# Optimization experiments

Measured on AMD Instinct MI355X. Metric: run time of the kernel, lower is better.

## Reference

```python
import jax, jax.numpy as jnp
import numpy as np

DIM = 2048
N_HEADS = 16
N_KV_HEADS = 4
HEAD_DIM = 128
EPS = 1e-6
BS, SEQ = 2, 4096


def setup_inputs() -> dict:
    key = jax.random.key(0)
    ks = jax.random.split(key, 8)
    x = jax.random.normal(ks[0], (BS, SEQ, DIM), dtype=jnp.float32)
    # rotary freqs: unit-modulus complex represented as [seq, head_dim//2, 2]
    theta = 10000.0
    inv_freq = 1.0 / (theta ** (jnp.arange(0, HEAD_DIM, 2, dtype=jnp.float32) / HEAD_DIM))
    t = jnp.arange(SEQ, dtype=jnp.float32)
    ang = jnp.outer(t, inv_freq)  # [SEQ, HEAD_DIM//2]
    freqs_cis = jnp.stack([jnp.cos(ang), jnp.sin(ang)], axis=-1)  # [SEQ, HD/2, 2]
    std = 0.02
    wq = jax.random.normal(ks[1], (N_HEADS * HEAD_DIM, DIM), dtype=jnp.float32) * std
    wk = jax.random.normal(ks[2], (N_KV_HEADS * HEAD_DIM, DIM), dtype=jnp.float32) * std
    wv = jax.random.normal(ks[3], (N_KV_HEADS * HEAD_DIM, DIM), dtype=jnp.float32) * std
    wo = jax.random.normal(ks[4], (DIM, N_HEADS * HEAD_DIM), dtype=jnp.float32) * std
    q_norm_w = jnp.ones((HEAD_DIM,), dtype=jnp.float32)
    k_norm_w = jnp.ones((HEAD_DIM,), dtype=jnp.float32)
    return {"x": x, "freqs_cis": freqs_cis, "wq": wq, "wk": wk, "wv": wv,
            "wo": wo, "q_norm_w": q_norm_w, "k_norm_w": k_norm_w}


def _rms_norm(x, w, eps=EPS):
    xf = x.astype(jnp.float32)
    var = jnp.mean(xf * xf, axis=-1, keepdims=True)
    return w * (xf * jax.lax.rsqrt(var + eps)).astype(x.dtype)


def _apply_rope(x, freqs_cis):
    # x: [b, s, h, d]; freqs_cis: [s, d//2, 2] (cos, sin)
    b, s, h, d = x.shape
    xr = x.astype(jnp.float32).reshape(b, s, h, d // 2, 2)
    cos = freqs_cis[:s, :, 0][None, :, None, :]
    sin = freqs_cis[:s, :, 1][None, :, None, :]
    xre, xim = xr[..., 0], xr[..., 1]
    out = jnp.stack([xre * cos - xim * sin, xre * sin + xim * cos], axis=-1)
    return out.reshape(b, s, h, d).astype(x.dtype)


def reference(x, freqs_cis, wq, wk, wv, wo, q_norm_w, k_norm_w):
    bs, seqlen, _ = x.shape
    xq = jnp.einsum('bsd,ed->bse', x, wq).reshape(bs, seqlen, N_HEADS, HEAD_DIM)
    xk = jnp.einsum('bsd,ed->bse', x, wk).reshape(bs, seqlen, N_KV_HEADS, HEAD_DIM)
    xv = jnp.einsum('bsd,ed->bse', x, wv).reshape(bs, seqlen, N_KV_HEADS, HEAD_DIM)
    xq = _rms_norm(xq, q_norm_w)
    xk = _rms_norm(xk, k_norm_w)
    xq = _apply_rope(xq, freqs_cis)
    xk = _apply_rope(xk, freqs_cis)
    n_rep = N_HEADS // N_KV_HEADS
    # repeat_kv: [b,s,kvh,d] -> [b,s,kvh*n_rep,d]
    keys = jnp.repeat(xk, n_rep, axis=2)
    values = jnp.repeat(xv, n_rep, axis=2)
    q = xq.transpose(0, 2, 1, 3)  # [b,h,s,d]
    k = keys.transpose(0, 2, 1, 3)
    v = values.transpose(0, 2, 1, 3)
    scale = 1.0 / jnp.sqrt(jnp.asarray(HEAD_DIM, dtype=q.dtype))
    scores = jnp.einsum('bhqd,bhkd->bhqk', q, k) * scale
    causal = jnp.tril(jnp.ones((seqlen, seqlen), dtype=bool))
    scores = jnp.where(causal[None, None], scores, jnp.finfo(scores.dtype).min)
    attn = jax.nn.softmax(scores, axis=-1)
    out = jnp.einsum('bhqk,bhkd->bhqd', attn, v)
    out = out.transpose(0, 2, 1, 3).reshape(bs, seqlen, N_HEADS * HEAD_DIM)
    return jnp.einsum('bse,de->bsd', out, wo)
```

## Files before the change

### kernel.cpp

```cpp
#include <hip/hip_runtime.h>

typedef __bf16 bf16;
typedef __bf16 bf16x8 __attribute__((ext_vector_type(8)));
typedef __bf16 bf16x4 __attribute__((ext_vector_type(4)));
typedef __bf16 bf16x2 __attribute__((ext_vector_type(2)));
typedef float  f32x4  __attribute__((ext_vector_type(4)));

static_assert(sizeof(bf16x8) == 16, "bf16x8 must be 16B");

#define MFMA16(a, b, c) __builtin_amdgcn_mfma_f32_16x16x32_bf16((a), (b), (c), 0, 0, 0)

__device__ __forceinline__ void gload_lds16(const void* g, void* l) {
    __builtin_amdgcn_global_load_lds(
        (const __attribute__((address_space(1))) void*)(uintptr_t)g,
        (__attribute__((address_space(3))) void*)(uintptr_t)l,
        16, 0, 0);
}

__device__ __forceinline__ void cast8(const float* __restrict__ in, bf16* __restrict__ out, int i)
{
    const float4 a = ((const float4*)in)[i * 2];
    const float4 b = ((const float4*)in)[i * 2 + 1];
    bf16x8 o;
    o[0] = (bf16)a.x; o[1] = (bf16)a.y; o[2] = (bf16)a.z; o[3] = (bf16)a.w;
    o[4] = (bf16)b.x; o[5] = (bf16)b.y; o[6] = (bf16)b.z; o[7] = (bf16)b.w;
    ((bf16x8*)out)[i] = o;
}

__global__ __launch_bounds__(256)
void cast_all(const float* __restrict__ x,  const float* __restrict__ wq,
              const float* __restrict__ wk, const float* __restrict__ wv,
              bf16* __restrict__ xb, bf16* __restrict__ wb)
{
    const int blk = blockIdx.x;
    if (blk < 8192) {
        cast8(x, xb, blk * 256 + threadIdx.x);
    } else if (blk < 10240) {
        cast8(wq, wb, (blk - 8192) * 256 + threadIdx.x);
    } else if (blk < 10752) {
        cast8(wk, wb + 2048 * 2048, (blk - 10240) * 256 + threadIdx.x);
    } else {
        cast8(wv, wb + 2560 * 2048, (blk - 10752) * 256 + threadIdx.x);
    }
}

template <typename OT, bool FUSE_VT>
__global__ __launch_bounds__(256)
void gemm_bt(const bf16* __restrict__ A, const bf16* __restrict__ W,
             int K, int ldc, OT* __restrict__ C, bf16* __restrict__ vTp)
{
    __shared__ bf16 smem[2 * 128 * 64];
    bf16* As = smem;
    bf16* Bs = smem + 128 * 64;

    const int n0 = blockIdx.x * 128;
    const int m0 = blockIdx.y * 128;

    const int tid  = threadIdx.x;
    const int lane = tid & 63;
    const int wid  = tid >> 6;
    const int wm   = wid >> 1;
    const int wn   = wid & 1;
    const int quad = lane >> 4;
    const int l16  = lane & 15;
    const int key  = l16 & 7;

    const int srow  = wid * 32 + (lane >> 3);
    const int scolg = ((lane & 7) ^ (lane >> 3)) * 8;
    const bf16* ag = A + (size_t)(m0 + srow) * K + scolg;
    const bf16* wg = W + (size_t)(n0 + srow) * K + scolg;
    bf16* al = As + wid * 2048;
    bf16* bl = Bs + wid * 2048;

    f32x4 acc[4][4];
#pragma unroll
    for (int i = 0; i < 4; i++)
#pragma unroll
        for (int j = 0; j < 4; j++) acc[i][j] = f32x4{0.f, 0.f, 0.f, 0.f};

    for (int kt = 0; kt < K; kt += 64) {
        __syncthreads();
#pragma unroll
        for (int i = 0; i < 4; i++) {
            gload_lds16(ag + (size_t)(i * 8) * K, al + i * 8 * 64);
            gload_lds16(wg + (size_t)(i * 8) * K, bl + i * 8 * 64);
        }
        ag += 64; wg += 64;
        __syncthreads();

#pragma unroll
        for (int ks = 0; ks < 2; ks++) {
            bf16x8 af[4], bfv[4];
#pragma unroll
            for (int i = 0; i < 4; i++)
                af[i]  = *(const bf16x8*)(As + (wm * 64 + i * 16 + l16) * 64 + (((ks * 4 + quad) ^ key) * 8));
#pragma unroll
            for (int i = 0; i < 4; i++)
                bfv[i] = *(const bf16x8*)(Bs + (wn * 64 + i * 16 + l16) * 64 + (((ks * 4 + quad) ^ key) * 8));
#pragma unroll
            for (int mi = 0; mi < 4; mi++)
#pragma unroll
                for (int ni = 0; ni < 4; ni++)
                    acc[mi][ni] = MFMA16(af[mi], bfv[ni], acc[mi][ni]);
        }
    }

    if (FUSE_VT && n0 >= 2560) {
        __syncthreads();
        bf16* T = smem;
#pragma unroll
        for (int mi = 0; mi < 4; mi++) {
            const int scol = wm * 64 + mi * 16 + quad * 4;
            const int g    = scol >> 3;
            const int sub  = scol & 7;
#pragma unroll
            for (int ni = 0; ni < 4; ni++) {
                const int d = wn * 64 + ni * 16 + l16;
                bf16x4 h4;
                h4[0] = (bf16)acc[mi][ni][0]; h4[1] = (bf16)acc[mi][ni][1];
                h4[2] = (bf16)acc[mi][ni][2]; h4[3] = (bf16)acc[mi][ni][3];
                *(bf16x4*)(&T[d * 128 + ((g ^ (d & 7)) * 8 + sub)]) = h4;
            }
        }
        __syncthreads();
        const int kvh = (n0 - 2560) >> 7;
        const int bb  = m0 >> 12;
        bf16* vdst = vTp + ((size_t)((bb * 4 + kvh) * 128)) * 4096 + (m0 & 4095);
#pragma unroll
        for (int i = 0; i < 8; i++) {
            const int d = wid * 32 + i * 4 + quad;
            const bf16x8 v = *(const bf16x8*)(&T[d * 128 + ((l16 ^ (d & 7)) * 8)]);
            *(bf16x8*)(vdst + (size_t)d * 4096 + l16 * 8) = v;
        }
        return;
    }

#pragma unroll
    for (int mi = 0; mi < 4; mi++) {
        const int row = m0 + wm * 64 + mi * 16 + quad * 4;
#pragma unroll
        for (int ni = 0; ni < 4; ni++) {
            const int col = n0 + wn * 64 + ni * 16 + l16;
#pragma unroll
            for (int r = 0; r < 4; r++)
                C[(size_t)(row + r) * ldc + col] = (OT)acc[mi][ni][r];
        }
    }
}

__global__ __launch_bounds__(256)
void normrope_wo(bf16* __restrict__ qkv, const float* __restrict__ fc,
                 const float* __restrict__ qw, const float* __restrict__ kw,
                 const float* __restrict__ wo, bf16* __restrict__ wob)
{
    if (blockIdx.x >= 40960) {
        cast8(wo, wob, (blockIdx.x - 40960) * 256 + threadIdx.x);
        return;
    }
    const int row  = blockIdx.x * 4 + (threadIdx.x >> 6);
    const int lane = threadIdx.x & 63;
    const int slot = row % 20;
    const int tok  = row / 20;
    const int s    = tok & 4095;

    const float* w; int off; float post;
    if (slot < 16) { off = slot * 128;               w = qw; post = 0.12751681555f; }
    else           { off = 2048 + (slot - 16) * 128; w = kw; post = 1.0f; }

    bf16* p = qkv + (size_t)tok * 3072 + off;

    bf16x2 v = *(const bf16x2*)(p + 2 * lane);
    float x0 = (float)v[0], x1 = (float)v[1];

    float ss = x0 * x0 + x1 * x1;
    ss += __shfl_xor(ss, 1);  ss += __shfl_xor(ss, 2);  ss += __shfl_xor(ss, 4);
    ss += __shfl_xor(ss, 8);  ss += __shfl_xor(ss, 16); ss += __shfl_xor(ss, 32);
    const float r = rsqrtf(ss * (1.0f / 128.0f) + 1e-6f) * post;

    const float xn0 = x0 * r * w[2 * lane], xn1 = x1 * r * w[2 * lane + 1];

    const float2 cs = ((const float2*)fc)[(size_t)s * 64 + lane];
    const float c = cs.x, sn = cs.y;

    bf16x2 o;
    o[0] = (bf16)(xn0 * c - xn1 * sn);
    o[1] = (bf16)(xn0 * sn + xn1 * c);
    *(bf16x2*)(p + 2 * lane) = o;
}

__global__ __launch_bounds__(256, 2)
void flash(const bf16* __restrict__ qkv, const bf16* __restrict__ vT,
           bf16* __restrict__ out)
{
    const int flat = blockIdx.y * 16 + blockIdx.x;
    const int xcd  = flat & 7;
    const int idx  = flat >> 3;
    const int b    = xcd >> 2;
    const int kvh  = xcd & 3;
    const int h    = kvh * 4 + (idx >> 4);
    const int bx   = idx & 15;

    const int tid  = threadIdx.x;
    const int lane = tid & 63;
    const int wid  = tid >> 6;
    const int quad = lane >> 4;
    const int l16  = lane & 15;
    const int key  = l16 & 7;

    __shared__ bf16 Ks[2][64 * 128];
    __shared__ bf16 Vs[128 * 64];
    __shared__ bf16 Ps[128 * 64];

    const bf16* kbase = qkv + (size_t)b * 4096 * 3072 + 2048 + kvh * 128;
    const bf16* vbase = vT + ((size_t)(b * 4 + kvh) * 128) * 4096;

    const int krow_off = lane >> 4;
    const int kcolg    = lane & 15;
    const int vrow_off = lane >> 3;
    const int vcolg    = lane & 7;

    for (int pass = 0; pass < 2; ++pass) {
        const int qt = pass ? (31 - bx) : bx;
        const int q0 = qt * 128;
        const int ntiles = qt * 2 + 2;

        __syncthreads();
#pragma unroll
        for (int i = 0; i < 4; i++) {
            const int r0 = wid * 16 + i * 4;
            const int rk = r0 + krow_off;
            const int gc = (kcolg ^ (rk & 7)) * 8;
            gload_lds16(kbase + (size_t)rk * 3072 + gc, &Ks[0][r0 * 128]);
        }

        bf16x8 qf[2][4];
        const bf16* qbase = qkv + ((size_t)(b * 4096 + q0 + wid * 32)) * 3072 + h * 128;
#pragma unroll
        for (int mt = 0; mt < 2; mt++)
#pragma unroll
            for (int ks = 0; ks < 4; ks++)
                qf[mt][ks] = *(const bf16x8*)(qbase + (size_t)(mt * 16 + l16) * 3072 + ks * 32 + quad * 8);

        f32x4 oacc[2][8];
#pragma unroll
        for (int mt = 0; mt < 2; mt++)
#pragma unroll
            for (int nd = 0; nd < 8; nd++) oacc[mt][nd] = f32x4{0.f, 0.f, 0.f, 0.f};
        float mrow[2], lrow[2];
#pragma unroll
        for (int mt = 0; mt < 2; mt++) { mrow[mt] = -__builtin_inff(); lrow[mt] = 0.f; }

        __syncthreads();

#pragma unroll
        for (int i = 0; i < 4; i++) {
            const int r0 = wid * 32 + i * 8;
            const int dv = r0 + vrow_off;
            const int gc = (vcolg ^ (dv & 7)) * 8;
            gload_lds16(vbase + (size_t)dv * 4096 + gc, &Vs[r0 * 64]);
        }
#pragma unroll
        for (int i = 0; i < 4; i++) {
            const int r0 = wid * 16 + i * 4;
            const int rk = r0 + krow_off;
            const int gc = (kcolg ^ (rk & 7)) * 8;
            gload_lds16(kbase + (size_t)(64 + rk) * 3072 + gc, &Ks[1][r0 * 128]);
        }

        f32x4 sA[2][4], sB[2][4];

        {
#pragma unroll
            for (int mt = 0; mt < 2; mt++)
#pragma unroll
                for (int nt = 0; nt < 4; nt++) sA[mt][nt] = f32x4{0.f, 0.f, 0.f, 0.f};
            __builtin_amdgcn_s_setprio(1);
#pragma unroll
            for (int ks = 0; ks < 4; ks++) {
                bf16x8 kf[4];
#pragma unroll
                for (int nt = 0; nt < 4; nt++)
                    kf[nt] = *(const bf16x8*)(&Ks[0][(nt * 16 + l16) * 128 + (((ks * 4 + quad) ^ key) * 8)]);
#pragma unroll
                for (int mt = 0; mt < 2; mt++)
#pragma unroll
                    for (int nt = 0; nt < 4; nt++)
                        sA[mt][nt] = MFMA16(kf[nt], qf[mt][ks], sA[mt][nt]);
            }
            __builtin_amdgcn_s_setprio(0);
        }

        auto step = [&](int t, f32x4 (&SA)[2][4], f32x4 (&SB)[2][4]) {
            const int kv0 = t * 64;

            if (kv0 + 63 > q0) {
#pragma unroll
                for (int mt = 0; mt < 2; mt++) {
                    const int qg = q0 + wid * 32 + mt * 16 + l16;
#pragma unroll
                    for (int nt = 0; nt < 4; nt++)
#pragma unroll
                        for (int r = 0; r < 4; r++) {
                            const int kvg = kv0 + nt * 16 + quad * 4 + r;
                            if (kvg > qg) SA[mt][nt][r] = -1e30f;
                        }
                }
            }

            float pm[2];
#pragma unroll
            for (int mt = 0; mt < 2; mt++) {
                float t8[8];
#pragma unroll
                for (int nt = 0; nt < 4; nt++) {
                    t8[2 * nt]     = fmaxf(SA[mt][nt][0], SA[mt][nt][1]);
                    t8[2 * nt + 1] = fmaxf(SA[mt][nt][2], SA[mt][nt][3]);
                }
                float m = fmaxf(fmaxf(fmaxf(t8[0], t8[1]), fmaxf(t8[2], t8[3])),
                                fmaxf(fmaxf(t8[4], t8[5]), fmaxf(t8[6], t8[7])));
                m = fmaxf(m, __shfl_xor(m, 16));
                m = fmaxf(m, __shfl_xor(m, 32));
                pm[mt] = m;
            }

            const bool rescale =
                !__all((pm[0] - mrow[0] <= 8.f) && (pm[1] - mrow[1] <= 8.f));
            if (rescale) {
#pragma unroll
                for (int mt = 0; mt < 2; mt++) {
                    const float mnew  = fmaxf(mrow[mt], pm[mt]);
                    const float alpha = exp2f(mrow[mt] - mnew);
                    mrow[mt] = mnew;
                    lrow[mt] *= alpha;
                    float ar[4];
#pragma unroll
                    for (int r = 0; r < 4; r++) ar[r] = __shfl(alpha, quad * 4 + r);
#pragma unroll
                    for (int nd = 0; nd < 8; nd++)
#pragma unroll
                        for (int r = 0; r < 4; r++) oacc[mt][nd][r] *= ar[r];
                }
            }

#pragma unroll
            for (int mt = 0; mt < 2; mt++) {
                const int prow = wid * 32 + mt * 16 + l16;
                float sn[4];
#pragma unroll
                for (int nt = 0; nt < 4; nt++) {
                    const float p0 = exp2f(SA[mt][nt][0] - mrow[mt]);
                    const float p1 = exp2f(SA[mt][nt][1] - mrow[mt]);
                    const float p2 = exp2f(SA[mt][nt][2] - mrow[mt]);
                    const float p3 = exp2f(SA[mt][nt][3] - mrow[mt]);
                    sn[nt] = (p0 + p1) + (p2 + p3);
                    bf16x4 h4;
                    h4[0] = (bf16)p0; h4[1] = (bf16)p1;
                    h4[2] = (bf16)p2; h4[3] = (bf16)p3;
                    const int g = (2 * nt + (quad >> 1)) ^ key;
                    *(bf16x4*)(&Ps[prow * 64 + g * 8 + (quad & 1) * 4]) = h4;
                }
                float s = (sn[0] + sn[1]) + (sn[2] + sn[3]);
                s += __shfl_xor(s, 16);
                s += __shfl_xor(s, 32);
                lrow[mt] += s;
            }

            __syncthreads();

            if (t + 1 < ntiles) {
#pragma unroll
                for (int mt = 0; mt < 2; mt++)
#pragma unroll
                    for (int nt = 0; nt < 4; nt++) SB[mt][nt] = f32x4{0.f, 0.f, 0.f, 0.f};
                __builtin_amdgcn_s_setprio(1);
#pragma unroll
                for (int ks = 0; ks < 4; ks++) {
                    bf16x8 kf[4];
#pragma unroll
                    for (int nt = 0; nt < 4; nt++)
                        kf[nt] = *(const bf16x8*)(&Ks[(t + 1) & 1][(nt * 16 + l16) * 128 + (((ks * 4 + quad) ^ key) * 8)]);
#pragma unroll
                    for (int mt = 0; mt < 2; mt++)
#pragma unroll
                        for (int nt = 0; nt < 4; nt++)
                            SB[mt][nt] = MFMA16(kf[nt], qf[mt][ks], SB[mt][nt]);
                }
                __builtin_amdgcn_s_setprio(0);
            }

            __builtin_amdgcn_s_setprio(1);
#pragma unroll
            for (int ks = 0; ks < 2; ks++) {
                bf16x8 pf[2];
#pragma unroll
                for (int mt = 0; mt < 2; mt++)
                    pf[mt] = *(const bf16x8*)(&Ps[(wid * 32 + mt * 16 + l16) * 64 + (((ks * 4 + quad) ^ key) * 8)]);
#pragma unroll
                for (int nd = 0; nd < 8; nd++) {
                    const bf16x8 vf = *(const bf16x8*)(&Vs[(nd * 16 + l16) * 64 + (((ks * 4 + quad) ^ key) * 8)]);
#pragma unroll
                    for (int mt = 0; mt < 2; mt++)
                        oacc[mt][nd] = MFMA16(pf[mt], vf, oacc[mt][nd]);
                }
            }
            __builtin_amdgcn_s_setprio(0);

            if (t + 1 < ntiles) {
                __syncthreads();
                const int kvv = (t + 1) * 64;
#pragma unroll
                for (int i = 0; i < 4; i++) {
                    const int r0 = wid * 32 + i * 8;
                    const int dv = r0 + vrow_off;
                    const int gc = (vcolg ^ (dv & 7)) * 8;
                    gload_lds16(vbase + (size_t)dv * 4096 + kvv + gc, &Vs[r0 * 64]);
                }
                if (t + 2 < ntiles) {
                    const int kvn = (t + 2) * 64;
#pragma unroll
                    for (int i = 0; i < 4; i++) {
                        const int r0 = wid * 16 + i * 4;
                        const int rk = r0 + krow_off;
                        const int gc = (kcolg ^ (rk & 7)) * 8;
                        gload_lds16(kbase + (size_t)(kvn + rk) * 3072 + gc, &Ks[t & 1][r0 * 128]);
                    }
                }
            }
        };

        for (int t = 0; t < ntiles; t += 2) {
            step(t,     sA, sB);
            step(t + 1, sB, sA);
        }

#pragma unroll
        for (int mt = 0; mt < 2; mt++) {
            const float inv = 1.0f / lrow[mt];
            float invr[4];
#pragma unroll
            for (int r = 0; r < 4; r++) invr[r] = __shfl(inv, quad * 4 + r);
#pragma unroll
            for (int r = 0; r < 4; r++) {
                const size_t srow = (size_t)(b * 4096 + q0 + wid * 32 + mt * 16 + quad * 4 + r);
#pragma unroll
                for (int nd = 0; nd < 8; nd++)
                    out[srow * 2048 + h * 128 + nd * 16 + l16] = (bf16)(oacc[mt][nd][r] * invr[r]);
            }
        }
    }
}

extern "C" void kernel_launch(void* const* d_in, const int* in_sizes, int n_in,
                              void* d_out, int out_size, void* d_ws, size_t ws_size,
                              hipStream_t stream)
{
    const float* x   = (const float*)d_in[0];
    const float* fc  = (const float*)d_in[1];
    const float* wq  = (const float*)d_in[2];
    const float* wk  = (const float*)d_in[3];
    const float* wv  = (const float*)d_in[4];
    const float* wo  = (const float*)d_in[5];
    const float* qnw = (const float*)d_in[6];
    const float* knw = (const float*)d_in[7];
    float* out = (float*)d_out;

    char* ws = (char*)d_ws;
    bf16* qkv = (bf16*)ws;
    bf16* vT  = (bf16*)(ws + 50331648);
    bf16* xb  = (bf16*)(ws + 58720256);
    bf16* att = xb;
    bf16* wb  = (bf16*)(ws + 92274688);
    bf16* wob = wb;

    cast_all<<<dim3(11264), 256, 0, stream>>>(x, wq, wk, wv, xb, wb);
    gemm_bt<bf16, true><<<dim3(24, 64), 256, 0, stream>>>(xb, wb, 2048, 3072, qkv, vT);
    normrope_wo<<<dim3(43008), 256, 0, stream>>>(qkv, fc, qnw, knw, wo, wob);
    flash<<<dim3(16, 32), 256, 0, stream>>>(qkv, vT, att);
    gemm_bt<float, false><<<dim3(16, 64), 256, 0, stream>>>(att, wob, 2048, 2048, out, nullptr);
}
```

Baseline: 596.5 us.

## Use 256x128 GEMM tiles with 512 threads and double-buffered LDS prefetch

The projection GEMMs now compute 256x128 output tiles with 8 waves per block. Shared memory is double-buffered so the next K-slice loads while MFMAs run on the current one, leaving one barrier per iteration. This hides global-load latency and reuses each B tile across twice as many rows. In exchange the block uses 96KB of LDS, which limits occupancy, and the fused V-transpose epilogue is rewritten for the wider tile.

```diff
diff --git a/kernel.cpp b/kernel.cpp
--- a/kernel.cpp
+++ b/kernel.cpp
@@ -45,16 +45,14 @@
 }
 
 template <typename OT, bool FUSE_VT>
-__global__ __launch_bounds__(256)
-void gemm_bt(const bf16* __restrict__ A, const bf16* __restrict__ W,
+__global__ __launch_bounds__(512, 2)
+void gemm256(const bf16* __restrict__ A, const bf16* __restrict__ W,
              int K, int ldc, OT* __restrict__ C, bf16* __restrict__ vTp)
 {
-    __shared__ bf16 smem[2 * 128 * 64];
-    bf16* As = smem;
-    bf16* Bs = smem + 128 * 64;
+    __shared__ bf16 smem[49152];
 
     const int n0 = blockIdx.x * 128;
-    const int m0 = blockIdx.y * 128;
+    const int m0 = blockIdx.y * 256;
 
     const int tid  = threadIdx.x;
     const int lane = tid & 63;
@@ -65,12 +63,8 @@
     const int l16  = lane & 15;
     const int key  = l16 & 7;
 
-    const int srow  = wid * 32 + (lane >> 3);
-    const int scolg = ((lane & 7) ^ (lane >> 3)) * 8;
-    const bf16* ag = A + (size_t)(m0 + srow) * K + scolg;
-    const bf16* wg = W + (size_t)(n0 + srow) * K + scolg;
-    bf16* al = As + wid * 2048;
-    bf16* bl = Bs + wid * 2048;
+    const int srow8 = lane >> 3;
+    const int sgran = lane & 7;
 
     f32x4 acc[4][4];
 #pragma unroll
@@ -78,16 +72,35 @@
 #pragma unroll
         for (int j = 0; j < 4; j++) acc[i][j] = f32x4{0.f, 0.f, 0.f, 0.f};
 
-    for (int kt = 0; kt < K; kt += 64) {
-        __syncthreads();
+    const int NT = K >> 6;
+
+    auto stage = [&](int kt, int bufi) {
+        bf16* da = smem + bufi * 24576;
+        bf16* db = da + 16384;
 #pragma unroll
         for (int i = 0; i < 4; i++) {
-            gload_lds16(ag + (size_t)(i * 8) * K, al + i * 8 * 64);
-            gload_lds16(wg + (size_t)(i * 8) * K, bl + i * 8 * 64);
-        }
-        ag += 64; wg += 64;
-        __syncthreads();
-
+            const int row = i * 64 + wid * 8 + srow8;
+            const int g   = sgran ^ (row & 7);
+            gload_lds16(A + (size_t)(m0 + row) * K + kt * 64 + g * 8,
+                        da + (i * 512 + wid * 64) * 8);
+        }
+#pragma unroll
+        for (int i = 0; i < 2; i++) {
+            const int row = i * 64 + wid * 8 + srow8;
+            const int g   = sgran ^ (row & 7);
+            gload_lds16(W + (size_t)(n0 + row) * K + kt * 64 + g * 8,
+                        db + (i * 512 + wid * 64) * 8);
+        }
+    };
+
+    stage(0, 0);
+    __syncthreads();
+
+    for (int kt = 0; kt < NT; kt++) {
+        if (kt + 1 < NT) stage(kt + 1, (kt + 1) & 1);
+
+        const bf16* As = smem + (kt & 1) * 24576;
+        const bf16* Bs = As + 16384;
 #pragma unroll
         for (int ks = 0; ks < 2; ks++) {
             bf16x8 af[4], bfv[4];
@@ -103,23 +116,23 @@
                 for (int ni = 0; ni < 4; ni++)
                     acc[mi][ni] = MFMA16(af[mi], bfv[ni], acc[mi][ni]);
         }
+        __syncthreads();
     }
 
     if (FUSE_VT && n0 >= 2560) {
-        __syncthreads();
         bf16* T = smem;
 #pragma unroll
         for (int mi = 0; mi < 4; mi++) {
-            const int scol = wm * 64 + mi * 16 + quad * 4;
-            const int g    = scol >> 3;
-            const int sub  = scol & 7;
+            const int sl  = wm * 64 + mi * 16 + quad * 4;
+            const int g   = sl >> 3;
+            const int sub = sl & 7;
 #pragma unroll
             for (int ni = 0; ni < 4; ni++) {
                 const int d = wn * 64 + ni * 16 + l16;
                 bf16x4 h4;
                 h4[0] = (bf16)acc[mi][ni][0]; h4[1] = (bf16)acc[mi][ni][1];
                 h4[2] = (bf16)acc[mi][ni][2]; h4[3] = (bf16)acc[mi][ni][3];
-                *(bf16x4*)(&T[d * 128 + ((g ^ (d & 7)) * 8 + sub)]) = h4;
+                *(bf16x4*)(&T[d * 256 + ((g ^ (d & 7)) * 8 + sub)]) = h4;
             }
         }
         __syncthreads();
@@ -128,9 +141,11 @@
         bf16* vdst = vTp + ((size_t)((bb * 4 + kvh) * 128)) * 4096 + (m0 & 4095);
 #pragma unroll
         for (int i = 0; i < 8; i++) {
-            const int d = wid * 32 + i * 4 + quad;
-            const bf16x8 v = *(const bf16x8*)(&T[d * 128 + ((l16 ^ (d & 7)) * 8)]);
-            *(bf16x8*)(vdst + (size_t)d * 4096 + l16 * 8) = v;
+            const int flat = i * 512 + tid;
+            const int d    = flat >> 5;
+            const int gr   = flat & 31;
+            const bf16x8 v = *(const bf16x8*)(&T[d * 256 + ((gr ^ (d & 7)) * 8)]);
+            *(bf16x8*)(vdst + (size_t)d * 4096 + gr * 8) = v;
         }
         return;
     }
@@ -473,8 +488,8 @@
     bf16* wob = wb;
 
     cast_all<<<dim3(11264), 256, 0, stream>>>(x, wq, wk, wv, xb, wb);
-    gemm_bt<bf16, true><<<dim3(24, 64), 256, 0, stream>>>(xb, wb, 2048, 3072, qkv, vT);
+    gemm256<bf16, true><<<dim3(24, 32), 512, 0, stream>>>(xb, wb, 2048, 3072, qkv, vT);
     normrope_wo<<<dim3(43008), 256, 0, stream>>>(qkv, fc, qnw, knw, wo, wob);
     flash<<<dim3(16, 32), 256, 0, stream>>>(qkv, vT, att);
-    gemm_bt<float, false><<<dim3(16, 64), 256, 0, stream>>>(att, wob, 2048, 2048, out, nullptr);
-}
+    gemm256<float, false><<<dim3(16, 32), 512, 0, stream>>>(att, wob, 2048, 2048, out, nullptr);
+}
```

Measured after the change: 562.5 us. 5.7% less time.
